# Optimization experiments

Hardware: AMD Instinct MI355X
Metric: run time of the kernel (lower is better)

The kernel has to match this reference:

```python
import jax, jax.numpy as jnp
import numpy as np

B, H, W, C = 32, 32, 32, 256
AD, RR = 8, 16
DN = ('NHWC', 'HWIO', 'NHWC')


def _conv(a, w, dil=1, groups=1):
    return jax.lax.conv_general_dilated(a, w, (1, 1), 'SAME', rhs_dilation=(dil, dil),
                                        dimension_numbers=DN, feature_group_count=groups)


def _branch(a, w1, b1, dw, pw, b3, wd, bd):
    # (Conv1x1 + SeparableConv3x3 + DilatedConv3x3), each sigmoid-activated, averaged
    y1 = jax.nn.sigmoid(_conv(a, w1) + b1)
    y3 = jax.nn.sigmoid(_conv(_conv(a, dw, groups=a.shape[-1]), pw) + b3)  # depthwise (no bias) -> pointwise
    yd = jax.nn.sigmoid(_conv(a, wd, dil=2) + bd)
    return (y1 + y3 + yd) / 3.0


def setup_inputs() -> dict:
    key = jax.random.key(0)
    ks = iter(jax.random.split(key, 64))
    nrm = lambda shape, s=0.05: jax.random.normal(next(ks), shape, jnp.float32) * s
    d = {'x': jax.random.normal(next(ks), (B, H, W, C), jnp.float32)}
    for p in ('cc', 'ch', 'cw'):
        d[p + '1_w'] = nrm((1, 1, C, 1)); d[p + '1_b'] = jnp.zeros((1,), jnp.float32)
        d[p + '3_dw'] = nrm((3, 3, 1, C)); d[p + '3_pw'] = nrm((1, 1, C, 1)); d[p + '3_b'] = jnp.zeros((1,), jnp.float32)
        d[p + 'd_w'] = nrm((3, 3, C, 1)); d[p + 'd_b'] = jnp.zeros((1,), jnp.float32)
    d['branch_w'] = jax.random.uniform(next(ks), (3,), jnp.float32, -0.05, 0.05)
    d['d1_w'] = nrm((C, RR)); d['d1_b'] = jnp.zeros((RR,), jnp.float32)
    d['d2_w'] = nrm((RR, 1)); d['d2_b'] = jnp.zeros((1,), jnp.float32)
    for p in ('q', 'k', 'v'):
        d[p + '_w'] = nrm((1, 1, 3, AD)); d[p + '_b'] = jnp.zeros((AD,), jnp.float32)
    d['o_w'] = nrm((1, 1, AD, 1)); d['o_b'] = jnp.zeros((1,), jnp.float32)
    d['gamma'] = jnp.ones((H, W, C), jnp.float32)
    d['beta'] = jnp.zeros((H, W, C), jnp.float32)
    return d


def reference(x, cc1_w, cc1_b, cc3_dw, cc3_pw, cc3_b, ccd_w, ccd_b,
              ch1_w, ch1_b, ch3_dw, ch3_pw, ch3_b, chd_w, chd_b,
              cw1_w, cw1_b, cw3_dw, cw3_pw, cw3_b, cwd_w, cwd_b,
              branch_w, d1_w, d1_b, d2_w, d2_b,
              q_w, q_b, k_w, k_b, v_w, v_b, o_w, o_b, gamma, beta):
    Bx, Hx, Wx, Cx = x.shape
    # global SE context: GAP -> Dense(relu) -> Dense(sigmoid) -> broadcast over H,W
    g = jnp.mean(x, axis=(1, 2), keepdims=True)                       # [B,1,1,C]
    g = jax.nn.relu(g @ d1_w + d1_b)
    g = jax.nn.sigmoid(g @ d2_w + d2_b)                               # [B,1,1,1]
    # channel branch: mean over H,W -> convs over [B,1,1,C] -> scalar gate
    ca = _branch(jnp.mean(x, axis=(1, 2), keepdims=True), cc1_w, cc1_b, cc3_dw, cc3_pw, cc3_b, ccd_w, ccd_b)  # [B,1,1,1]
    x_c = x * ca
    # height branch: mean over W -> [B,1,H,C] -> convs -> [B,1,H,1] -> gate per-H
    ha_in = jnp.transpose(jnp.mean(x, axis=2, keepdims=True), (0, 2, 1, 3))
    ha = _branch(ha_in, ch1_w, ch1_b, ch3_dw, ch3_pw, ch3_b, chd_w, chd_b)
    x_h = x * jnp.transpose(ha, (0, 2, 1, 3))                         # [B,H,1,1] broadcast
    # width branch: mean over H -> [B,1,W,C] -> convs -> [B,1,W,1] -> gate per-W
    wa = _branch(jnp.mean(x, axis=1, keepdims=True), cw1_w, cw1_b, cw3_dw, cw3_pw, cw3_b, cwd_w, cwd_b)
    x_w = x * wa
    bw = jax.nn.softmax(branch_w)
    combined = bw[0] * x_c + bw[1] * x_h + bw[2] * x_w
    # small self-attention over the 3 channel-mean maps
    maps = jnp.concatenate([jnp.mean(x_c, axis=-1, keepdims=True),
                            jnp.mean(x_h, axis=-1, keepdims=True),
                            jnp.mean(x_w, axis=-1, keepdims=True)], axis=-1)  # [B,H,W,3]
    Q = (jnp.einsum('bhwc,co->bhwo', maps, q_w[0, 0]) + q_b).reshape(Bx, Hx * Wx, AD)
    K = (jnp.einsum('bhwc,co->bhwo', maps, k_w[0, 0]) + k_b).reshape(Bx, Hx * Wx, AD)
    V = (jnp.einsum('bhwc,co->bhwo', maps, v_w[0, 0]) + v_b).reshape(Bx, Hx * Wx, AD)
    att = jax.nn.softmax(jnp.einsum('bnd,bmd->bnm', Q, K) / jnp.sqrt(jnp.float32(AD)), axis=-1)
    ao = jnp.einsum('bnm,bmd->bnd', att, V).reshape(Bx, Hx, Wx, AD)
    cross = jax.nn.sigmoid(jnp.einsum('bhwd,do->bhwo', ao, o_w[0, 0]) + o_b)  # [B,H,W,1]
    y = combined * cross * g + x
    # LayerNorm over (H,W,C) per sample, keras eps=1e-3
    mu = jnp.mean(y, axis=(1, 2, 3), keepdims=True)
    var = jnp.mean((y - mu) ** 2, axis=(1, 2, 3), keepdims=True)
    return (y - mu) / jnp.sqrt(var + 1e-3) * gamma + beta
```

## Files before the change

### kernel.cpp

```cpp
#include <hip/hip_runtime.h>


#define B_   32
#define H_   32
#define W_   32
#define C_   256
#define N_   1024
#define HWC_ (32*32*256)

#define OFF_XW    0
#define OFF_XH    262144
#define OFF_MC    524288
#define OFF_M2    557056
#define OFF_T     589824
#define OFF_HA    622592
#define OFF_WA    623616
#define OFF_CA    624640
#define OFF_G     624672
#define OFF_CST   624704
#define OFF_LNP   624736
#define WS_FLOATS 626784

__device__ __forceinline__ float sigm_(float v){ return 1.f/(1.f + __expf(-v)); }

__global__ __launch_bounds__(256) void kAB(const float* __restrict__ x, float* __restrict__ ws){
  __shared__ float4 sl4[256];
  const int blk = blockIdx.x;
  const int tid = threadIdx.x, lane = tid & 63, wv = tid >> 6;
  if (blk < 1024){
    const int b = blk >> 5, h = blk & 31;
    const float* xp = x + (size_t)(b*H_ + h)*(W_*C_);
    float4 v[8];
    #pragma unroll
    for (int k = 0; k < 8; ++k) v[k] = ((const float4*)xp)[tid + k*256];
    #pragma unroll
    for (int k = 0; k < 8; ++k){
      float s = v[k].x + v[k].y + v[k].z + v[k].w;
      float q = v[k].x*v[k].x + v[k].y*v[k].y + v[k].z*v[k].z + v[k].w*v[k].w;
      #pragma unroll
      for (int d = 1; d < 64; d <<= 1){ s += __shfl_xor(s, d); q += __shfl_xor(q, d); }
      if (lane == 0){
        const int w = k*4 + wv;
        ws[OFF_MC + b*N_ + h*W_ + w] = s * (1.f/C_);
        ws[OFF_M2 + b*N_ + h*W_ + w] = q;
      }
    }
    float4 a = v[0];
    #pragma unroll
    for (int k = 1; k < 8; ++k){ a.x += v[k].x; a.y += v[k].y; a.z += v[k].z; a.w += v[k].w; }
    sl4[tid] = a;
    __syncthreads();
    if (tid < 64){
      const float4 p0 = sl4[tid], p1 = sl4[tid+64], p2 = sl4[tid+128], p3 = sl4[tid+192];
      float4 o;
      o.x = (p0.x+p1.x+p2.x+p3.x)*(1.f/W_);
      o.y = (p0.y+p1.y+p2.y+p3.y)*(1.f/W_);
      o.z = (p0.z+p1.z+p2.z+p3.z)*(1.f/W_);
      o.w = (p0.w+p1.w+p2.w+p3.w)*(1.f/W_);
      ((float4*)(ws + OFF_XW + (b*H_ + h)*C_))[tid] = o;
    }
  } else {
    const int blk2 = blk - 1024, b = blk2 >> 5, w = blk2 & 31;
    const int hh = tid >> 6, c4 = (tid & 63)*4;
    const float* xp = x + (size_t)b*HWC_ + (size_t)w*C_ + c4;
    float4 acc = {0.f,0.f,0.f,0.f};
    #pragma unroll
    for (int hb = 0; hb < 8; ++hb){
      const int h = hb*4 + hh;
      const float4 v = *(const float4*)(xp + (size_t)h*(W_*C_));
      acc.x += v.x; acc.y += v.y; acc.z += v.z; acc.w += v.w;
    }
    sl4[tid] = acc;
    __syncthreads();
    if (tid < 64){
      const float4 a = sl4[tid], b2 = sl4[tid+64], c = sl4[tid+128], d = sl4[tid+192];
      float4 o;
      o.x = (a.x+b2.x+c.x+d.x)*(1.f/H_);
      o.y = (a.y+b2.y+c.y+d.y)*(1.f/H_);
      o.z = (a.z+b2.z+c.z+d.z)*(1.f/H_);
      o.w = (a.w+b2.w+c.w+d.w)*(1.f/H_);
      *(float4*)&ws[OFF_XH + (b*W_ + w)*C_ + tid*4] = o;
    }
  }
}

__device__ __forceinline__ void branch_1d(const float* __restrict__ Xs, float* __restrict__ outg,
    const float* __restrict__ w1, const float* __restrict__ b1,
    const float* __restrict__ dw, const float* __restrict__ pw, const float* __restrict__ b3,
    const float* __restrict__ wd, const float* __restrict__ bd, int lane, int wave)
{
  for (int i = 0; i < 8; ++i){
    const int h = wave*8 + i;
    float s1 = 0.f, s3 = 0.f, sd = 0.f;
    #pragma unroll
    for (int k = 0; k < 4; ++k){
      const int c = lane + k*64;
      const float x0  = Xs[h*C_ + c];
      const float xm1 = (h > 0)  ? Xs[(h-1)*C_ + c] : 0.f;
      const float xp1 = (h < 31) ? Xs[(h+1)*C_ + c] : 0.f;
      const float xm2 = (h > 1)  ? Xs[(h-2)*C_ + c] : 0.f;
      const float xp2 = (h < 30) ? Xs[(h+2)*C_ + c] : 0.f;
      s1 = fmaf(x0, w1[c], s1);
      const float dv = xm1*dw[3*C_+c] + x0*dw[4*C_+c] + xp1*dw[5*C_+c];
      s3 = fmaf(dv, pw[c], s3);
      sd += xm2*wd[3*C_+c] + x0*wd[4*C_+c] + xp2*wd[5*C_+c];
    }
    #pragma unroll
    for (int d = 1; d < 64; d <<= 1){ s1 += __shfl_xor(s1,d); s3 += __shfl_xor(s3,d); sd += __shfl_xor(sd,d); }
    if (lane == 0)
      outg[h] = (sigm_(s1 + b1[0]) + sigm_(s3 + b3[0]) + sigm_(sd + bd[0])) * (1.f/3.f);
  }
}

__global__ __launch_bounds__(256) void kC(float* __restrict__ ws,
  const float* __restrict__ cc1_w, const float* __restrict__ cc1_b, const float* __restrict__ cc3_dw,
  const float* __restrict__ cc3_pw, const float* __restrict__ cc3_b, const float* __restrict__ ccd_w, const float* __restrict__ ccd_b,
  const float* __restrict__ ch1_w, const float* __restrict__ ch1_b, const float* __restrict__ ch3_dw,
  const float* __restrict__ ch3_pw, const float* __restrict__ ch3_b, const float* __restrict__ chd_w, const float* __restrict__ chd_b,
  const float* __restrict__ cw1_w, const float* __restrict__ cw1_b, const float* __restrict__ cw3_dw,
  const float* __restrict__ cw3_pw, const float* __restrict__ cw3_b, const float* __restrict__ cwd_w, const float* __restrict__ cwd_b,
  const float* __restrict__ branch_w, const float* __restrict__ d1_w, const float* __restrict__ d1_b,
  const float* __restrict__ d2_w, const float* __restrict__ d2_b,
  const float* __restrict__ q_w, const float* __restrict__ q_b, const float* __restrict__ k_w, const float* __restrict__ k_b,
  const float* __restrict__ v_w, const float* __restrict__ v_b, const float* __restrict__ o_w, const float* __restrict__ o_b)
{
  __shared__ float Xs[H_*C_];
  __shared__ float gvec[C_];
  const int b = blockIdx.x, part = blockIdx.y;
  const int tid = threadIdx.x, lane = tid & 63, wave = tid >> 6;

  if (part == 1){
    const float4* src = (const float4*)(ws + OFF_XH + b*(W_*C_));
    #pragma unroll
    for (int k = 0; k < 8; ++k) ((float4*)Xs)[tid + k*256] = src[tid + k*256];
    __syncthreads();
    branch_1d(Xs, ws + OFF_WA + b*32, cw1_w, cw1_b, cw3_dw, cw3_pw, cw3_b, cwd_w, cwd_b, lane, wave);
    return;
  }

  const float4* src = (const float4*)(ws + OFF_XW + b*(H_*C_));
  #pragma unroll
  for (int k = 0; k < 8; ++k) ((float4*)Xs)[tid + k*256] = src[tid + k*256];
  __syncthreads();
  { float s = 0.f;
    #pragma unroll
    for (int h = 0; h < H_; ++h) s += Xs[h*C_ + tid];
    gvec[tid] = s * (1.f/H_); }
  __syncthreads();

  branch_1d(Xs, ws + OFF_HA + b*32, ch1_w, ch1_b, ch3_dw, ch3_pw, ch3_b, chd_w, chd_b, lane, wave);

  if (wave == 0){
    float s1 = 0.f, s3 = 0.f, sd = 0.f;
    #pragma unroll
    for (int k = 0; k < 4; ++k){
      const int c = lane + k*64;
      const float v = gvec[c];
      s1 = fmaf(v, cc1_w[c], s1);
      s3 = fmaf(v*cc3_dw[4*C_+c], cc3_pw[c], s3);
      sd = fmaf(v, ccd_w[4*C_+c], sd);
    }
    #pragma unroll
    for (int d = 1; d < 64; d <<= 1){ s1 += __shfl_xor(s1,d); s3 += __shfl_xor(s3,d); sd += __shfl_xor(sd,d); }
    if (lane == 0)
      ws[OFF_CA + b] = (sigm_(s1+cc1_b[0]) + sigm_(s3+cc3_b[0]) + sigm_(sd+ccd_b[0])) * (1.f/3.f);
  } else if (wave == 1){
    float acc = 0.f;
    for (int r = 0; r < 16; ++r){
      float s = 0.f;
      #pragma unroll
      for (int k = 0; k < 4; ++k){ const int c = lane + k*64; s = fmaf(gvec[c], d1_w[c*16 + r], s); }
      #pragma unroll
      for (int d = 1; d < 64; d <<= 1) s += __shfl_xor(s, d);
      acc = fmaf(fmaxf(s + d1_b[r], 0.f), d2_w[r], acc);
    }
    if (lane == 0) ws[OFF_G + b] = sigm_(acc + d2_b[0]);
  } else if (wave == 2 && b == 0){
    if (lane < 16){
      const int i = lane >> 2, j = lane & 3;
      float s = 0.f;
      #pragma unroll
      for (int d = 0; d < 8; ++d){
        const float qv = (i < 3) ? q_w[i*8+d] : q_b[d];
        const float kv = (j < 3) ? k_w[j*8+d] : k_b[d];
        s = fmaf(qv, kv, s);
      }
      ws[OFF_CST + i*4 + j] = s * 0.51010305898f;
    } else if (lane < 19){
      const int i = lane - 16;
      float s = 0.f;
      #pragma unroll
      for (int d = 0; d < 8; ++d) s = fmaf(v_w[i*8+d], o_w[d], s);
      ws[OFF_CST + lane] = s;
    } else if (lane == 19){
      float s = o_b[0];
      #pragma unroll
      for (int d = 0; d < 8; ++d) s = fmaf(v_b[d], o_w[d], s);
      ws[OFF_CST + 19] = s;
    } else if (lane == 20){
      const float b0 = branch_w[0], b1 = branch_w[1], b2 = branch_w[2];
      const float mx = fmaxf(b0, fmaxf(b1, b2));
      const float e0 = __expf(b0-mx), e1 = __expf(b1-mx), e2 = __expf(b2-mx);
      const float inv = 1.f/(e0+e1+e2);
      ws[OFF_CST+20] = e0*inv; ws[OFF_CST+21] = e1*inv; ws[OFF_CST+22] = e2*inv;
      ws[OFF_CST+23] = 0.f;
    }
  }
}

#define ATT1(MV, WV) do{                       \
    const float vv = fmaf(p2, (WV), th);       \
    const float ss = fmaf((MV), vv, p3);       \
    const float ee = exp2f(ss);                \
    Z += ee;                                   \
    const float em = ee * (MV);                \
    semc += em;                                \
    A2 = fmaf(em, (WV), A2);                   \
  }while(0)

__global__ __launch_bounds__(256) void kD(float* __restrict__ ws){
  __shared__ __align__(16) float mcs[4*1032];
  __shared__ float ha_s[32], wa_s[32], cst[24], sc[2], red[8];
  const int blk = blockIdx.x, b = blk >> 5, rblk = blk & 31;
  const int tid = threadIdx.x, lane = tid & 63, wv = tid >> 6;
  {
    const float4 v = ((const float4*)(ws + OFF_MC + b*N_))[tid];
    #pragma unroll
    for (int cp = 0; cp < 4; ++cp) *(float4*)&mcs[cp*1032 + tid*4] = v;
  }
  if (tid < 32){ ha_s[tid] = ws[OFF_HA + b*32 + tid]; wa_s[tid] = ws[OFF_WA + b*32 + tid]; }
  else if (tid >= 64 && tid < 88) cst[tid-64] = ws[OFF_CST + (tid-64)];
  else if (tid == 96){ sc[0] = ws[OFF_CA + b]; sc[1] = ws[OFF_G + b]; }
  __syncthreads();

  const float ca = sc[0], gg = sc[1];
  const int r = tid >> 3, sub = tid & 7;
  const int n = rblk*32 + r;
  const int hn = n >> 5, wn = n & 31;
  const float mcn = mcs[n];
  const float u0 = mcn*ca, u1 = mcn*ha_s[hn], u2 = mcn*wa_s[wn];
  const float p0 = u0*cst[0] + u1*cst[4] + u2*cst[8]  + cst[12];
  const float p1 = u0*cst[1] + u1*cst[5] + u2*cst[9]  + cst[13];
  const float p2 = u0*cst[2] + u1*cst[6] + u2*cst[10] + cst[14];
  const float p3 = u0*cst[3] + u1*cst[7] + u2*cst[11] + cst[15];
  const float pc = p0 * ca;

  float Z = 0.f, A0 = 0.f, A1 = 0.f, A2 = 0.f;
  const float* mrow_base = &mcs[(sub & 3)*1032];
  #pragma unroll
  for (int i = 0; i < 4; ++i){
    const int hm = sub*4 + i;
    const float th = fmaf(p1, ha_s[hm], pc);
    float semc = 0.f;
    const float* mrow = mrow_base + hm*32;
    #pragma unroll
    for (int wm = 0; wm < 32; wm += 4){
      const float4 m4 = *(const float4*)&mrow[wm];
      const float4 w4 = *(const float4*)&wa_s[wm];
      ATT1(m4.x, w4.x);
      ATT1(m4.y, w4.y);
      ATT1(m4.z, w4.z);
      ATT1(m4.w, w4.w);
    }
    A0 += semc; A1 = fmaf(ha_s[hm], semc, A1);
  }
  #pragma unroll
  for (int d = 1; d < 8; d <<= 1){
    Z  += __shfl_xor(Z, d);
    A0 += __shfl_xor(A0, d);
    A1 += __shfl_xor(A1, d);
    A2 += __shfl_xor(A2, d);
  }

  float t1 = 0.f, t2 = 0.f;
  if (sub == 0){
    const float invZ = 1.f / Z;
    const float dot = (ca*cst[16]*A0 + cst[17]*A1 + cst[18]*A2) * invZ + cst[19];
    const float cross = 1.f / (1.f + __expf(-dot));
    const float S = cst[20]*ca + cst[21]*ha_s[hn] + cst[22]*wa_s[wn];
    const float T = fmaf(S*cross, gg, 1.f);
    ws[OFF_T + b*N_ + n] = T;
    t1 = T * mcn * (float)C_;
    t2 = T * T * ws[OFF_M2 + b*N_ + n];
  }
  #pragma unroll
  for (int d = 1; d < 64; d <<= 1){ t1 += __shfl_xor(t1,d); t2 += __shfl_xor(t2,d); }
  if (lane == 0){ red[wv] = t1; red[4+wv] = t2; }
  __syncthreads();
  if (tid == 0){
    ws[OFF_LNP + (b*32 + rblk)*2 + 0] = red[0]+red[1]+red[2]+red[3];
    ws[OFF_LNP + (b*32 + rblk)*2 + 1] = red[4]+red[5]+red[6]+red[7];
  }
}

__global__ __launch_bounds__(256) void kF(const float* __restrict__ x, const float* __restrict__ gamma,
                                          const float* __restrict__ beta, const float* __restrict__ ws,
                                          float* __restrict__ out){
  const int blk = blockIdx.x, b = blk >> 5, h = blk & 31;
  const int tid = threadIdx.x;
  __shared__ float a1s[32];
  __shared__ float mu_r[2];
  if (tid == 0){
    float s1 = 0.f, s2 = 0.f;
    for (int i = 0; i < 32; ++i){
      s1 += ws[OFF_LNP + (b*32+i)*2 + 0];
      s2 += ws[OFF_LNP + (b*32+i)*2 + 1];
    }
    const float mu  = s1 * (1.f/HWC_);
    const float var = s2 * (1.f/HWC_) - mu*mu;
    const float rstd = rsqrtf(var + 1e-3f);
    mu_r[0] = mu * rstd; mu_r[1] = rstd;
  }
  __syncthreads();
  if (tid < 32) a1s[tid] = ws[OFF_T + b*N_ + h*32 + tid] * mu_r[1];
  __syncthreads();
  const float murstd = mu_r[0];
  const size_t base = (size_t)(b*H_ + h)*(W_*C_);
  const float4* xp = (const float4*)(x + base);
  const float4* gp = (const float4*)(gamma + (size_t)h*(W_*C_));
  const float4* bp = (const float4*)(beta  + (size_t)h*(W_*C_));
  float4* op = (float4*)(out + base);
  #pragma unroll
  for (int k = 0; k < 8; ++k){
    const int f = tid + k*256;
    const float a1 = a1s[f >> 6];
    const float4 xv = xp[f], gv = gp[f], bv = bp[f];
    float4 o;
    o.x = fmaf(fmaf(xv.x, a1, -murstd), gv.x, bv.x);
    o.y = fmaf(fmaf(xv.y, a1, -murstd), gv.y, bv.y);
    o.z = fmaf(fmaf(xv.z, a1, -murstd), gv.z, bv.z);
    o.w = fmaf(fmaf(xv.w, a1, -murstd), gv.w, bv.w);
    op[f] = o;
  }
}

extern "C" void kernel_launch(void* const* d_in, const int* in_sizes, int n_in,
                              void* d_out, int out_size, void* d_ws, size_t ws_size,
                              hipStream_t stream){
  (void)in_sizes; (void)n_in; (void)out_size;
  if (ws_size < (size_t)WS_FLOATS * sizeof(float)) return;
  const float* x      = (const float*)d_in[0];
  const float* cc1_w  = (const float*)d_in[1];
  const float* cc1_b  = (const float*)d_in[2];
  const float* cc3_dw = (const float*)d_in[3];
  const float* cc3_pw = (const float*)d_in[4];
  const float* cc3_b  = (const float*)d_in[5];
  const float* ccd_w  = (const float*)d_in[6];
  const float* ccd_b  = (const float*)d_in[7];
  const float* ch1_w  = (const float*)d_in[8];
  const float* ch1_b  = (const float*)d_in[9];
  const float* ch3_dw = (const float*)d_in[10];
  const float* ch3_pw = (const float*)d_in[11];
  const float* ch3_b  = (const float*)d_in[12];
  const float* chd_w  = (const float*)d_in[13];
  const float* chd_b  = (const float*)d_in[14];
  const float* cw1_w  = (const float*)d_in[15];
  const float* cw1_b  = (const float*)d_in[16];
  const float* cw3_dw = (const float*)d_in[17];
  const float* cw3_pw = (const float*)d_in[18];
  const float* cw3_b  = (const float*)d_in[19];
  const float* cwd_w  = (const float*)d_in[20];
  const float* cwd_b  = (const float*)d_in[21];
  const float* branch_w = (const float*)d_in[22];
  const float* d1_w   = (const float*)d_in[23];
  const float* d1_b   = (const float*)d_in[24];
  const float* d2_w   = (const float*)d_in[25];
  const float* d2_b   = (const float*)d_in[26];
  const float* q_w    = (const float*)d_in[27];
  const float* q_b    = (const float*)d_in[28];
  const float* k_w    = (const float*)d_in[29];
  const float* k_b    = (const float*)d_in[30];
  const float* v_w    = (const float*)d_in[31];
  const float* v_b    = (const float*)d_in[32];
  const float* o_w    = (const float*)d_in[33];
  const float* o_b    = (const float*)d_in[34];
  const float* gamma  = (const float*)d_in[35];
  const float* beta   = (const float*)d_in[36];
  float* ws = (float*)d_ws;
  float* out = (float*)d_out;

  kAB<<<dim3(2048), dim3(256), 0, stream>>>(x, ws);
  kC<<<dim3(B_, 2), dim3(256), 0, stream>>>(ws,
      cc1_w, cc1_b, cc3_dw, cc3_pw, cc3_b, ccd_w, ccd_b,
      ch1_w, ch1_b, ch3_dw, ch3_pw, ch3_b, chd_w, chd_b,
      cw1_w, cw1_b, cw3_dw, cw3_pw, cw3_b, cwd_w, cwd_b,
      branch_w, d1_w, d1_b, d2_w, d2_b,
      q_w, q_b, k_w, k_b, v_w, v_b, o_w, o_b);
  kD<<<dim3(B_*32), dim3(256), 0, stream>>>(ws);
  kF<<<dim3(B_*H_), dim3(256), 0, stream>>>(x, gamma, beta, ws, out);
}
```

Before: 52.96 us.

## Split kC branch conv work across 16 extra blocks per batch, one row per wave

The 1-D branch convolutions for the H and W profiles previously ran in one or two blocks per sample, staged through 32 KB of shared memory, with each wave looping over 8 rows. Now the grid has 17 blocks per sample: 16 blocks give each wave a single row and read the neighbouring rows straight from global memory as float4. The remaining block only computes the global channel mean and the SE and attention constants. This raises parallelism and occupancy in the small kC stage and drops the large shared-memory staging, at the cost of redundant global reads of neighbouring rows and weights.

```diff
diff --git a/kernel.cpp b/kernel.cpp
--- a/kernel.cpp
+++ b/kernel.cpp
@@ -22,6 +22,9 @@
 #define WS_FLOATS 626784
 
 __device__ __forceinline__ float sigm_(float v){ return 1.f/(1.f + __expf(-v)); }
+__device__ __forceinline__ float dot4_(float4 a, float4 b){
+  return a.x*b.x + a.y*b.y + a.z*b.z + a.w*b.w;
+}
 
 __global__ __launch_bounds__(256) void kAB(const float* __restrict__ x, float* __restrict__ ws){
   __shared__ float4 sl4[256];
@@ -81,34 +84,6 @@
       o.w = (a.w+b2.w+c.w+d.w)*(1.f/H_);
       *(float4*)&ws[OFF_XH + (b*W_ + w)*C_ + tid*4] = o;
     }
-  }
-}
-
-__device__ __forceinline__ void branch_1d(const float* __restrict__ Xs, float* __restrict__ outg,
-    const float* __restrict__ w1, const float* __restrict__ b1,
-    const float* __restrict__ dw, const float* __restrict__ pw, const float* __restrict__ b3,
-    const float* __restrict__ wd, const float* __restrict__ bd, int lane, int wave)
-{
-  for (int i = 0; i < 8; ++i){
-    const int h = wave*8 + i;
-    float s1 = 0.f, s3 = 0.f, sd = 0.f;
-    #pragma unroll
-    for (int k = 0; k < 4; ++k){
-      const int c = lane + k*64;
-      const float x0  = Xs[h*C_ + c];
-      const float xm1 = (h > 0)  ? Xs[(h-1)*C_ + c] : 0.f;
-      const float xp1 = (h < 31) ? Xs[(h+1)*C_ + c] : 0.f;
-      const float xm2 = (h > 1)  ? Xs[(h-2)*C_ + c] : 0.f;
-      const float xp2 = (h < 30) ? Xs[(h+2)*C_ + c] : 0.f;
-      s1 = fmaf(x0, w1[c], s1);
-      const float dv = xm1*dw[3*C_+c] + x0*dw[4*C_+c] + xp1*dw[5*C_+c];
-      s3 = fmaf(dv, pw[c], s3);
-      sd += xm2*wd[3*C_+c] + x0*wd[4*C_+c] + xp2*wd[5*C_+c];
-    }
-    #pragma unroll
-    for (int d = 1; d < 64; d <<= 1){ s1 += __shfl_xor(s1,d); s3 += __shfl_xor(s3,d); sd += __shfl_xor(sd,d); }
-    if (lane == 0)
-      outg[h] = (sigm_(s1 + b1[0]) + sigm_(s3 + b3[0]) + sigm_(sd + bd[0])) * (1.f/3.f);
   }
 }
 
@@ -124,33 +99,63 @@
   const float* __restrict__ q_w, const float* __restrict__ q_b, const float* __restrict__ k_w, const float* __restrict__ k_b,
   const float* __restrict__ v_w, const float* __restrict__ v_b, const float* __restrict__ o_w, const float* __restrict__ o_b)
 {
-  __shared__ float Xs[H_*C_];
+  const int b = blockIdx.x, y = blockIdx.y;
+  const int tid = threadIdx.x, lane = tid & 63, wv = tid >> 6;
+
+  if (y < 16){
+    const int prof = y >> 3;
+    const int h = ((y & 7) << 2) | wv;
+    const float* P  = ws + (prof ? OFF_XH : OFF_XW) + b*(32*C_);
+    const float* w1 = prof ? cw1_w  : ch1_w;
+    const float* b1 = prof ? cw1_b  : ch1_b;
+    const float* dw = prof ? cw3_dw : ch3_dw;
+    const float* pw = prof ? cw3_pw : ch3_pw;
+    const float* b3 = prof ? cw3_b  : ch3_b;
+    const float* wd = prof ? cwd_w  : chd_w;
+    const float* bd = prof ? cwd_b  : chd_b;
+    const int c4 = lane*4;
+    const float4 z4 = {0.f,0.f,0.f,0.f};
+    const float4 r0  = *(const float4*)(P + h*C_ + c4);
+    const float4 rm1 = (h > 0)  ? *(const float4*)(P + (h-1)*C_ + c4) : z4;
+    const float4 rp1 = (h < 31) ? *(const float4*)(P + (h+1)*C_ + c4) : z4;
+    const float4 rm2 = (h > 1)  ? *(const float4*)(P + (h-2)*C_ + c4) : z4;
+    const float4 rp2 = (h < 30) ? *(const float4*)(P + (h+2)*C_ + c4) : z4;
+    const float4 w1q = *(const float4*)(w1 + c4);
+    const float4 d3  = *(const float4*)(dw + 3*C_ + c4);
+    const float4 d4  = *(const float4*)(dw + 4*C_ + c4);
+    const float4 d5  = *(const float4*)(dw + 5*C_ + c4);
+    const float4 pwq = *(const float4*)(pw + c4);
+    const float4 g3  = *(const float4*)(wd + 3*C_ + c4);
+    const float4 g4  = *(const float4*)(wd + 4*C_ + c4);
+    const float4 g5  = *(const float4*)(wd + 5*C_ + c4);
+    float s1 = dot4_(r0, w1q);
+    float4 dv;
+    dv.x = rm1.x*d3.x + r0.x*d4.x + rp1.x*d5.x;
+    dv.y = rm1.y*d3.y + r0.y*d4.y + rp1.y*d5.y;
+    dv.z = rm1.z*d3.z + r0.z*d4.z + rp1.z*d5.z;
+    dv.w = rm1.w*d3.w + r0.w*d4.w + rp1.w*d5.w;
+    float s3 = dot4_(dv, pwq);
+    float sd = (rm2.x*g3.x + r0.x*g4.x + rp2.x*g5.x)
+             + (rm2.y*g3.y + r0.y*g4.y + rp2.y*g5.y)
+             + (rm2.z*g3.z + r0.z*g4.z + rp2.z*g5.z)
+             + (rm2.w*g3.w + r0.w*g4.w + rp2.w*g5.w);
+    #pragma unroll
+    for (int d = 1; d < 64; d <<= 1){ s1 += __shfl_xor(s1,d); s3 += __shfl_xor(s3,d); sd += __shfl_xor(sd,d); }
+    if (lane == 0)
+      ws[(prof ? OFF_WA : OFF_HA) + b*32 + h] =
+          (sigm_(s1 + b1[0]) + sigm_(s3 + b3[0]) + sigm_(sd + bd[0])) * (1.f/3.f);
+    return;
+  }
+
   __shared__ float gvec[C_];
-  const int b = blockIdx.x, part = blockIdx.y;
-  const int tid = threadIdx.x, lane = tid & 63, wave = tid >> 6;
-
-  if (part == 1){
-    const float4* src = (const float4*)(ws + OFF_XH + b*(W_*C_));
-    #pragma unroll
-    for (int k = 0; k < 8; ++k) ((float4*)Xs)[tid + k*256] = src[tid + k*256];
-    __syncthreads();
-    branch_1d(Xs, ws + OFF_WA + b*32, cw1_w, cw1_b, cw3_dw, cw3_pw, cw3_b, cwd_w, cwd_b, lane, wave);
-    return;
-  }
-
-  const float4* src = (const float4*)(ws + OFF_XW + b*(H_*C_));
-  #pragma unroll
-  for (int k = 0; k < 8; ++k) ((float4*)Xs)[tid + k*256] = src[tid + k*256];
-  __syncthreads();
   { float s = 0.f;
-    #pragma unroll
-    for (int h = 0; h < H_; ++h) s += Xs[h*C_ + tid];
+    const float* P = ws + OFF_XW + b*(32*C_);
+    #pragma unroll
+    for (int h = 0; h < H_; ++h) s += P[h*C_ + tid];
     gvec[tid] = s * (1.f/H_); }
   __syncthreads();
 
-  branch_1d(Xs, ws + OFF_HA + b*32, ch1_w, ch1_b, ch3_dw, ch3_pw, ch3_b, chd_w, chd_b, lane, wave);
-
-  if (wave == 0){
+  if (wv == 0){
     float s1 = 0.f, s3 = 0.f, sd = 0.f;
     #pragma unroll
     for (int k = 0; k < 4; ++k){
@@ -164,7 +169,7 @@
     for (int d = 1; d < 64; d <<= 1){ s1 += __shfl_xor(s1,d); s3 += __shfl_xor(s3,d); sd += __shfl_xor(sd,d); }
     if (lane == 0)
       ws[OFF_CA + b] = (sigm_(s1+cc1_b[0]) + sigm_(s3+cc3_b[0]) + sigm_(sd+ccd_b[0])) * (1.f/3.f);
-  } else if (wave == 1){
+  } else if (wv == 1){
     float acc = 0.f;
     for (int r = 0; r < 16; ++r){
       float s = 0.f;
@@ -175,7 +180,7 @@
       acc = fmaf(fmaxf(s + d1_b[r], 0.f), d2_w[r], acc);
     }
     if (lane == 0) ws[OFF_G + b] = sigm_(acc + d2_b[0]);
-  } else if (wave == 2 && b == 0){
+  } else if (wv == 2 && b == 0){
     if (lane < 16){
       const int i = lane >> 2, j = lane & 3;
       float s = 0.f;
@@ -380,7 +385,7 @@
   float* out = (float*)d_out;
 
   kAB<<<dim3(2048), dim3(256), 0, stream>>>(x, ws);
-  kC<<<dim3(B_, 2), dim3(256), 0, stream>>>(ws,
+  kC<<<dim3(B_, 17), dim3(256), 0, stream>>>(ws,
       cc1_w, cc1_b, cc3_dw, cc3_pw, cc3_b, ccd_w, ccd_b,
       ch1_w, ch1_b, ch3_dw, ch3_pw, ch3_b, chd_w, chd_b,
       cw1_w, cw1_b, cw3_dw, cw3_pw, cw3_b, cwd_w, cwd_b,
```

Result: faster. 49.01 us (-7.5%).
